# Kernel optimization log

Measured on AMD Instinct MI355X. Metric: run time of the kernel, lower is better.

The kernel has to match this reference:

```python
import jax, jax.numpy as jnp
import numpy as np
import math

PE_DIM = 96
MAX_LEN = 150

def make_pe():
    # deterministic sinusoidal position embedding buffer (requires_grad=False in torch)
    pe = np.zeros((MAX_LEN, PE_DIM), np.float32)
    pos = np.arange(MAX_LEN, dtype=np.float32)[:, None]
    div = np.exp(np.arange(0, PE_DIM, 2, dtype=np.float32) * (-math.log(10000.0) / PE_DIM))
    pe[:, 0::2] = np.sin(pos * div)
    pe[:, 1::2] = np.cos(pos * div)
    return jnp.asarray(pe)

def gru_cell(x, h, Wih, Whh, bih, bhh):
    # PyTorch GRU cell semantics
    gi = x @ Wih.T + bih            # [B, 3H]
    gh = h @ Whh.T + bhh            # [B, 3H]
    ir, iz, in_ = jnp.split(gi, 3, axis=-1)
    hr, hz, hn = jnp.split(gh, 3, axis=-1)
    r = jax.nn.sigmoid(ir + hr)
    z = jax.nn.sigmoid(iz + hz)
    n = jnp.tanh(in_ + r * hn)
    return (1.0 - z) * n + z * h

def gru_step(x, h, params):
    # x: [B, in], h: [L, B, H] -> (top-layer out [B,H], new h [L,B,H])
    hs = []
    inp = x
    for l, (Wih, Whh, bih, bhh) in enumerate(params):
        hn = gru_cell(inp, h[l], Wih, Whh, bih, bhh)
        hs.append(hn)
        inp = hn
    return inp, jnp.stack(hs)

def setup_inputs() -> dict:
    key = jax.random.key(0)
    ks = jax.random.split(key, 12)
    T, B, F, H = 50, 256, 96, 512
    rnn_in = 2 * F + PE_DIM  # 288
    k = 1.0 / math.sqrt(H)
    u = lambda kk, shp: jax.random.uniform(kk, shp, jnp.float32, -k, k)
    return {
        'input': jax.random.normal(ks[0], (T, B, F), jnp.float32),
        'W_ih0': u(ks[1], (3 * H, rnn_in)), 'W_hh0': u(ks[2], (3 * H, H)),
        'b_ih0': u(ks[3], (3 * H,)), 'b_hh0': u(ks[4], (3 * H,)),
        'W_ih1': u(ks[5], (3 * H, H)), 'W_hh1': u(ks[6], (3 * H, H)),
        'b_ih1': u(ks[7], (3 * H,)), 'b_hh1': u(ks[8], (3 * H,)),
        'W_lin': u(ks[9], (F, H)), 'b_lin': u(ks[10], (F,)),
    }

def reference(input, W_ih0, W_hh0, b_ih0, b_hh0, W_ih1, W_hh1, b_ih1, b_hh1, W_lin, b_lin):
    pe = make_pe()
    params = [(W_ih0, W_hh0, b_ih0, b_hh0), (W_ih1, W_hh1, b_ih1, b_hh1)]
    T, B, F = input.shape
    H = W_hh0.shape[1]
    # std mask: torch.std over time (unbiased) > 1e-4, shape [1,B,F]
    mask = (jnp.std(input, axis=0, ddof=1, keepdims=True) > 1e-4).astype(input.dtype)
    # ---- encoder ----
    vel = jnp.concatenate([jnp.zeros((1, B, F), input.dtype), input[1:] - input[:-1]], 0)
    pos = jnp.broadcast_to(pe[:T, None, :], (T, B, PE_DIM))
    x_en = jnp.concatenate([input, vel, pos], -1)  # [T,B,288]
    h0 = jnp.zeros((2, B, H), input.dtype)
    def enc_step(h, xt):
        out, hn = gru_step(xt, h, params)
        return hn, out
    h_en, outs = jax.lax.scan(enc_step, h0, x_en)
    outputs_enc = outs @ W_lin.T + b_lin + input  # residual: pred_pre = input
    pe_dec = pe[T:2 * T]  # step i uses pe[T+i]
    m = mask[0]
    def dec_core(prev_pred, vel_t, pe_t, h):
        x = jnp.concatenate([prev_pred, vel_t,
                             jnp.broadcast_to(pe_t[None, :], (B, PE_DIM))], -1)
        out, hn = gru_step(x, h, params)
        pred = (out @ W_lin.T + b_lin + prev_pred) * m  # residual then std_mask
        return pred, hn
    # step 0: input[0] with velocity input[0]-input[-1], hidden from encoder
    pred0, h = dec_core(input[0], input[0] - input[-1], pe_dec[0], h_en)
    # steps >=1: inp_cur = pred, and pred - outputs_dec[i-1] == 0 (faithful to source)
    zero_vel = jnp.zeros((B, F), input.dtype)
    def dec_step(carry, pe_t):
        pred, h = carry
        pred_n, hn = dec_core(pred, zero_vel, pe_t, h)
        return (pred_n, hn), pred_n
    _, preds = jax.lax.scan(dec_step, (pred0, h), pe_dec[1:])
    outputs_dec = jnp.concatenate([pred0[None], preds], 0)
    return (outputs_enc, outputs_dec)
```

## Files before the change

### kernel.cpp

```cpp
#include <hip/hip_runtime.h>
#include <math.h>

#define TT 50
#define BB 256
#define FF 96
#define HH 512
#define G3 1536
#define RNN_IN 288
#define HSZ (BB * HH)

typedef __attribute__((ext_vector_type(8))) short bhalf8;
typedef __attribute__((ext_vector_type(4))) float floatx4;
#define MFMA16 __builtin_amdgcn_mfma_f32_16x16x32_bf16

__device__ inline ushort f2bf(float f) {
    union { float f; unsigned u; } v; v.f = f;
    unsigned r = (v.u + 0x7FFFu + ((v.u >> 16) & 1u)) >> 16;
    return (ushort)r;
}
__device__ inline float bf2f(ushort h) {
    union { unsigned u; float f; } v; v.u = ((unsigned)h) << 16; return v.f;
}
__device__ inline bhalf8 ld8(const ushort* p) { return *(const bhalf8*)p; }
__device__ inline float sigmoidf_(float x) { return 1.f / (1.f + __expf(-x)); }

__device__ inline float pe_val(int pos, int d) {
    float dv = expf(-9.210340371976184f * (float)(d & ~1) / 96.0f);
    float a = (float)pos * dv;
    return (d & 1) ? cosf(a) : sinf(a);
}

__global__ __launch_bounds__(256) void prep_weights(
    const float* Wih0, const float* Whh0, const float* Wih1, const float* Whh1, const float* Wlin,
    ushort* dWih0, ushort* dWhh0, ushort* dWih1, ushort* dWhh1, ushort* dWlin)
{
    const int n0 = G3 * RNN_IN;
    const int n1 = G3 * HH;
    const int n2 = FF * HH;
    const int total = n0 + 3 * n1 + n2;
    for (int i = blockIdx.x * 256 + threadIdx.x; i < total; i += gridDim.x * 256) {
        int j = i;
        if (j < n0) { dWih0[j] = f2bf(Wih0[j]); continue; }
        j -= n0;
        if (j < n1) { dWhh0[j] = f2bf(Whh0[j]); continue; }
        j -= n1;
        if (j < n1) { dWih1[j] = f2bf(Wih1[j]); continue; }
        j -= n1;
        if (j < n1) { dWhh1[j] = f2bf(Whh1[j]); continue; }
        j -= n1;
        dWlin[j] = f2bf(Wlin[j]);
    }
}

__global__ __launch_bounds__(256) void prep_misc(
    const float* __restrict__ input, float* pe, float* maskp, ushort* x_en,
    ushort* hb, unsigned* bar)
{
    int i = blockIdx.x * 256 + threadIdx.x;
    if (i < TT * BB * RNN_IN) {
        int t = i / (BB * RNN_IN);
        int r = i % (BB * RNN_IN);
        int b = r / RNN_IN, c = r % RNN_IN;
        float v;
        if (c < FF) v = input[(t * BB + b) * FF + c];
        else if (c < 2 * FF) {
            int cc = c - FF;
            v = (t == 0) ? 0.f : input[(t * BB + b) * FF + cc] - input[((t - 1) * BB + b) * FF + cc];
        } else v = pe_val(t, c - 2 * FF);
        x_en[i] = f2bf(v);
        return;
    }
    i -= TT * BB * RNN_IN;
    if (i < BB * FF) {
        int b = i / FF, f = i % FF;
        float mean = 0.f, sq = 0.f;
        for (int t = 0; t < TT; t++) {
            float x = input[(t * BB + b) * FF + f];
            mean += x; sq += x * x;
        }
        mean /= (float)TT;
        float var = (sq - (float)TT * mean * mean) / (float)(TT - 1);
        float sd = sqrtf(fmaxf(var, 0.f));
        maskp[i] = (sd > 1e-4f) ? 1.f : 0.f;
        return;
    }
    i -= BB * FF;
    if (i < 100 * FF) { pe[i] = pe_val(i / FF, i % FF); return; }
    i -= 100 * FF;
    if (i < 4 * BB * HH) { hb[i] = 0; return; }
    i -= 4 * BB * HH;
    if (i < 16384) { bar[i] = 0; return; }
}

__global__ __launch_bounds__(256) void zpe_kernel(
    const float* __restrict__ pe, const float* __restrict__ Wih0,
    const float* __restrict__ bih0, float* __restrict__ Zpe)
{
    int idx = blockIdx.x * 256 + threadIdx.x;
    if (idx >= TT * G3) return;
    int t = idx / G3, n = idx % G3;
    float s = bih0[n];
    const float* per = pe + (TT + t) * FF;
    const float* wr = Wih0 + n * RNN_IN + 2 * FF;
    for (int k = 0; k < FF; k++) s += per[k] * wr[k];
    Zpe[idx] = s;
}

__global__ __launch_bounds__(256) void zvel_kernel(
    const float* __restrict__ input, const float* __restrict__ Wih0, float* __restrict__ Zvel)
{
    int idx = blockIdx.x * 256 + threadIdx.x;
    if (idx >= BB * G3) return;
    int m = idx / G3, n = idx % G3;
    const float* a0 = input + m * FF;
    const float* aL = input + (TT - 1) * BB * FF + m * FF;
    const float* wr = Wih0 + n * RNN_IN;
    float s = 0.f;
    for (int k = 0; k < FF; k++) s += a0[k] * wr[k] + (a0[k] - aL[k]) * wr[FF + k];
    Zvel[idx] = s;
}

__global__ __launch_bounds__(256) void gemm_z0(
    const ushort* __restrict__ A, const ushort* __restrict__ W,
    const float* __restrict__ bias, ushort* __restrict__ C)
{
    int lane = threadIdx.x & 63, w = threadIdx.x >> 6;
    int row0 = blockIdx.x * 64 + w * 16;
    int c0 = blockIdx.y * 96;
    int l15 = lane & 15, q = lane >> 4;
    const ushort* ap = A + (size_t)(row0 + l15) * RNN_IN + q * 8;
    floatx4 acc[6] = {};
    const ushort* wp[6];
#pragma unroll
    for (int j = 0; j < 6; j++) wp[j] = W + (size_t)(c0 + 16 * j + l15) * RNN_IN + q * 8;
    for (int kt = 0; kt < RNN_IN / 32; kt++) {
        bhalf8 a = ld8(ap + kt * 32);
#pragma unroll
        for (int j = 0; j < 6; j++) {
            bhalf8 b = ld8(wp[j] + kt * 32);
            acc[j] = MFMA16(a, b, acc[j], 0, 0, 0);
        }
    }
#pragma unroll
    for (int j = 0; j < 6; j++) {
        int col = c0 + 16 * j + l15;
        float bb = bias[col];
#pragma unroll
        for (int i = 0; i < 4; i++) {
            int r = row0 + q * 4 + i;
            C[(size_t)r * G3 + col] = f2bf(acc[j][i] + bb);
        }
    }
}

__global__ __launch_bounds__(256) void gemm_out_enc(
    const ushort* __restrict__ A, const ushort* __restrict__ W,
    const float* __restrict__ bias, const float* __restrict__ addsrc, float* __restrict__ out)
{
    int lane = threadIdx.x & 63, w = threadIdx.x >> 6;
    int row0 = blockIdx.x * 64 + w * 16;
    int l15 = lane & 15, q = lane >> 4;
    const ushort* ap = A + (size_t)(row0 + l15) * HH + q * 8;
    floatx4 acc[6] = {};
    const ushort* wp[6];
#pragma unroll
    for (int j = 0; j < 6; j++) wp[j] = W + (size_t)(16 * j + l15) * HH + q * 8;
    for (int kt = 0; kt < HH / 32; kt++) {
        bhalf8 a = ld8(ap + kt * 32);
#pragma unroll
        for (int j = 0; j < 6; j++) {
            bhalf8 b = ld8(wp[j] + kt * 32);
            acc[j] = MFMA16(a, b, acc[j], 0, 0, 0);
        }
    }
#pragma unroll
    for (int j = 0; j < 6; j++) {
        int col = 16 * j + l15;
        float bb = bias[col];
#pragma unroll
        for (int i = 0; i < 4; i++) {
            int r = row0 + q * 4 + i;
            out[(size_t)r * FF + col] = acc[j][i] + bb + addsrc[(size_t)r * FF + col];
        }
    }
}


struct PArgs {
    const ushort* Z0;
    const ushort* Wih0b;
    const ushort* Whh0b; const ushort* Wih1b; const ushort* Whh1b;
    const ushort* Wlinb;
    const float* bhh0; const float* bih1; const float* bhh1; const float* blin;
    const float* Zpe;
    const float* Zvel;
    const float* maskp;
    const float* input;
    ushort* h0buf;
    ushort* h1buf;
    ushort* outs;
    float* out;
    unsigned* slots;
};

__global__ __launch_bounds__(128) void persistent11(PArgs P)
{
    const int tid = threadIdx.x;
    const int w = tid >> 6;
    const int lane = tid & 63;
    const int l15 = lane & 15, q = lane >> 4;
    const int rg = blockIdx.x >> 4, cg = blockIdx.x & 15;
    const int row0 = rg * 16;
    const int ct = cg * 32 + w * 16;
    const int bcol = ct + q * 4;
    const int lcol = w * 16 + q * 4;

    __shared__ ushort h0stage[8192];
    __shared__ ushort h1stage[8192];
    __shared__ float h0f[16][36];
    __shared__ float h1f[16][36];
    __shared__ float predf[16][100];
    __shared__ float maskl[16][100];
    __shared__ ushort predb[16][104];

    for (int i = tid; i < 16 * 36; i += 128) { ((float*)h0f)[i] = 0.f; ((float*)h1f)[i] = 0.f; }
    for (int i = tid; i < 16 * 96; i += 128) {
        int r = i / 96, c = i % 96;
        float p0 = P.input[(row0 + r) * FF + c];
        predf[r][c] = p0;
        predb[r][c] = f2bf(p0);
        maskl[r][c] = P.maskp[(row0 + r) * FF + c];
    }
    __syncthreads();

    unsigned phase = 0;
    unsigned* myslot = P.slots + (size_t)(rg * 16 + cg) * 64;
    const unsigned* pslot = P.slots + (size_t)(rg * 16 + (tid & 15)) * 64;

    auto release = [&]() {
        phase++;
        asm volatile("s_waitcnt vmcnt(0)" ::: "memory");
        __syncthreads();
        if (tid == 0)
            __hip_atomic_store(myslot, phase, __ATOMIC_RELAXED, __HIP_MEMORY_SCOPE_AGENT);
    };
    auto wait_ = [&]() {
        if (tid < 16 && tid != cg) {
            while (__hip_atomic_load(pslot, __ATOMIC_RELAXED, __HIP_MEMORY_SCOPE_AGENT) < phase)
                __builtin_amdgcn_s_sleep(1);
        }
        __syncthreads();
        asm volatile("" ::: "memory");
    };

    auto stage = [&](const ushort* src, ushort* dst) {
        const int r = tid & 15;
        const int cb = tid >> 4;
        const unsigned long long* gp =
            (const unsigned long long*)(src + (size_t)(row0 + r) * HH + cb * 64);
        unsigned long long v[16];
#pragma unroll
        for (int j = 0; j < 16; j++)
            v[j] = __hip_atomic_load(gp + j, __ATOMIC_RELAXED, __HIP_MEMORY_SCOPE_AGENT);
#pragma unroll
        for (int qq = 0; qq < 8; qq++) {
            unsigned long long* lp = (unsigned long long*)(dst + ((cb * 8 + qq) * 16 + r) * 8);
            lp[0] = v[2 * qq];
            lp[1] = v[2 * qq + 1];
        }
    };

    auto gemm3_lds = [&](const ushort* hst, const ushort* W, floatx4 acc[3]) {
        const ushort* a0 = W + (size_t)(0 * HH + ct + l15) * HH + q * 8;
        const ushort* a1 = W + (size_t)(1 * HH + ct + l15) * HH + q * 8;
        const ushort* a2 = W + (size_t)(2 * HH + ct + l15) * HH + q * 8;
        for (int kt = 0; kt < 16; kt++) {
            bhalf8 b = *(const bhalf8*)&hst[((kt * 4 + q) * 16 + l15) * 8];
            acc[0] = MFMA16(ld8(a0), b, acc[0], 0, 0, 0); a0 += 32;
            acc[1] = MFMA16(ld8(a1), b, acc[1], 0, 0, 0); a1 += 32;
            acc[2] = MFMA16(ld8(a2), b, acc[2], 0, 0, 0); a2 += 32;
        }
    };

    auto gru_epi = [&](const floatx4 gi[3], const floatx4 gh[3], const float* bhh,
                       float (*hfl)[36], ushort* hnb, ushort* outs_t) {
        float4 bh_r = *(const float4*)&bhh[0 * HH + bcol];
        float4 bh_z = *(const float4*)&bhh[1 * HH + bcol];
        float4 bh_n = *(const float4*)&bhh[2 * HH + bcol];
        union { ushort s4[4]; unsigned long long u; } pk;
        const float* bhr = &bh_r.x; const float* bhz = &bh_z.x; const float* bhn = &bh_n.x;
#pragma unroll
        for (int i = 0; i < 4; i++) {
            float rg_ = sigmoidf_(gi[0][i] + gh[0][i] + bhr[i]);
            float zg = sigmoidf_(gi[1][i] + gh[1][i] + bhz[i]);
            float ng = tanhf(gi[2][i] + rg_ * (gh[2][i] + bhn[i]));
            float hn = (1.f - zg) * ng + zg * hfl[l15][lcol + i];
            hfl[l15][lcol + i] = hn;
            pk.s4[i] = f2bf(hn);
        }
        __hip_atomic_store((unsigned long long*)(hnb + (size_t)(row0 + l15) * HH + bcol), pk.u,
                           __ATOMIC_RELAXED, __HIP_MEMORY_SCOPE_AGENT);
        if (outs_t) *(unsigned long long*)(outs_t + (size_t)(row0 + l15) * HH + bcol) = pk.u;
    };

    auto pred_part = [&](int tpred) {
        float* outt = P.out + (size_t)(TT + tpred) * BB * FF;
        for (int jt = w; jt < 6; jt += 2) {
            floatx4 pa = {};
            const ushort* apw = P.Wlinb + (size_t)(jt * 16 + l15) * HH + q * 8;
            for (int kt = 0; kt < 16; kt++) {
                bhalf8 b = *(const bhalf8*)&h1stage[((kt * 4 + q) * 16 + l15) * 8];
                pa = MFMA16(ld8(apw), b, pa, 0, 0, 0); apw += 32;
            }
            int fc = jt * 16 + q * 4;
            float4 bl = *(const float4*)&P.blin[fc];
            const float* blp = &bl.x;
            float4 vout;
            float* vo = &vout.x;
#pragma unroll
            for (int i = 0; i < 4; i++) {
                float v = pa[i] + blp[i] + predf[l15][fc + i];
                v *= maskl[l15][fc + i];
                predf[l15][fc + i] = v;
                predb[l15][fc + i] = f2bf(v);
                vo[i] = v;
            }
            if (cg == 0) *(float4*)&outt[(size_t)(row0 + l15) * FF + fc] = vout;
        }
    };

    for (int s = 0; s <= TT; s++) {
        release();
        floatx4 gh1[3] = {};
        floatx4 gi0z[3];
        if (s >= 1) {
            stage(P.h1buf + (1 - (s & 1)) * HSZ, h1stage);
            __syncthreads();
            gemm3_lds(h1stage, P.Whh1b, gh1);
        }
        if (s < TT) {
            const ushort* zt = P.Z0 + ((size_t)s * BB + row0 + l15) * G3;
#pragma unroll
            for (int g = 0; g < 3; g++) {
                union { unsigned long long u; ushort s4[4]; } z;
                z.u = *(const unsigned long long*)(zt + g * HH + bcol);
#pragma unroll
                for (int i = 0; i < 4; i++) gi0z[g][i] = bf2f(z.s4[i]);
            }
        }
        wait_();
        stage(P.h0buf + (s & 1) * HSZ, h0stage);
        __syncthreads();
        if (s < TT) {
            floatx4 gh0[3] = {};
            gemm3_lds(h0stage, P.Whh0b, gh0);
            gru_epi(gi0z, gh0, P.bhh0, h0f, P.h0buf + (1 - (s & 1)) * HSZ, nullptr);
        }
        if (s >= 1) {
            int t = s - 1;
            floatx4 gi1[3] = {};
            gemm3_lds(h0stage, P.Wih1b, gi1);
            float4 bi0 = *(const float4*)&P.bih1[0 * HH + bcol];
            float4 bi1 = *(const float4*)&P.bih1[1 * HH + bcol];
            float4 bi2 = *(const float4*)&P.bih1[2 * HH + bcol];
            const float* b0 = &bi0.x; const float* b1 = &bi1.x; const float* b2 = &bi2.x;
#pragma unroll
            for (int i = 0; i < 4; i++) { gi1[0][i] += b0[i]; gi1[1][i] += b1[i]; gi1[2][i] += b2[i]; }
            gru_epi(gi1, gh1, P.bhh1, h1f, P.h1buf + (s & 1) * HSZ, P.outs + (size_t)t * BB * HH);
        }
    }

    for (int t = 0; t < TT; t++) {
        int pp = t & 1;
        release();
        stage(P.h0buf + pp * HSZ, h0stage);
        __syncthreads();
        floatx4 gh0[3] = {};
        gemm3_lds(h0stage, P.Whh0b, gh0);
        floatx4 zadd[3];
        {
            const float* zp = P.Zpe + (size_t)t * G3;
#pragma unroll
            for (int g = 0; g < 3; g++) {
                float4 z4 = *(const float4*)&zp[g * HH + bcol];
                const float* zp4 = &z4.x;
#pragma unroll
                for (int i = 0; i < 4; i++) zadd[g][i] = zp4[i];
            }
            if (t == 0) {
                const float* zv = P.Zvel + (size_t)(row0 + l15) * G3;
#pragma unroll
                for (int g = 0; g < 3; g++) {
                    float4 z4 = *(const float4*)&zv[g * HH + bcol];
                    const float* zp4 = &z4.x;
#pragma unroll
                    for (int i = 0; i < 4; i++) zadd[g][i] += zp4[i];
                }
            }
        }
        wait_();
        stage(P.h1buf + pp * HSZ, h1stage);
        __syncthreads();
        if (t > 0) {
            pred_part(t - 1);
            __syncthreads();
        }
        {
            floatx4 gi0[3] = {};
            if (t > 0) {
                const ushort* a0 = P.Wih0b + (size_t)(0 * HH + ct + l15) * RNN_IN + q * 8;
                const ushort* a1 = P.Wih0b + (size_t)(1 * HH + ct + l15) * RNN_IN + q * 8;
                const ushort* a2 = P.Wih0b + (size_t)(2 * HH + ct + l15) * RNN_IN + q * 8;
                for (int kt = 0; kt < 3; kt++) {
                    bhalf8 b = *(const bhalf8*)(&predb[l15][kt * 32 + q * 8]);
                    gi0[0] = MFMA16(ld8(a0), b, gi0[0], 0, 0, 0); a0 += 32;
                    gi0[1] = MFMA16(ld8(a1), b, gi0[1], 0, 0, 0); a1 += 32;
                    gi0[2] = MFMA16(ld8(a2), b, gi0[2], 0, 0, 0); a2 += 32;
                }
            }
#pragma unroll
            for (int g = 0; g < 3; g++)
#pragma unroll
                for (int i = 0; i < 4; i++) gi0[g][i] += zadd[g][i];
            gru_epi(gi0, gh0, P.bhh0, h0f, P.h0buf + (1 - pp) * HSZ, nullptr);
        }

        release();
        floatx4 gh1[3] = {};
        gemm3_lds(h1stage, P.Whh1b, gh1);
        wait_();
        stage(P.h0buf + (1 - pp) * HSZ, h0stage);
        __syncthreads();
        {
            floatx4 gi1[3] = {};
            gemm3_lds(h0stage, P.Wih1b, gi1);
            float4 bi0 = *(const float4*)&P.bih1[0 * HH + bcol];
            float4 bi1 = *(const float4*)&P.bih1[1 * HH + bcol];
            float4 bi2 = *(const float4*)&P.bih1[2 * HH + bcol];
            const float* b0 = &bi0.x; const float* b1 = &bi1.x; const float* b2 = &bi2.x;
#pragma unroll
            for (int i = 0; i < 4; i++) { gi1[0][i] += b0[i]; gi1[1][i] += b1[i]; gi1[2][i] += b2[i]; }
            gru_epi(gi1, gh1, P.bhh1, h1f, P.h1buf + (1 - pp) * HSZ, nullptr);
        }
    }
    release();
    wait_();
    stage(P.h1buf + 0 * HSZ, h1stage);
    __syncthreads();
    pred_part(TT - 1);
}

extern "C" void kernel_launch(void* const* d_in, const int* in_sizes, int n_in,
                              void* d_out, int out_size, void* d_ws, size_t ws_size,
                              hipStream_t stream)
{
    const float* input = (const float*)d_in[0];
    const float* W_ih0 = (const float*)d_in[1];
    const float* W_hh0 = (const float*)d_in[2];
    const float* b_ih0 = (const float*)d_in[3];
    const float* b_hh0 = (const float*)d_in[4];
    const float* W_ih1 = (const float*)d_in[5];
    const float* W_hh1 = (const float*)d_in[6];
    const float* b_ih1 = (const float*)d_in[7];
    const float* b_hh1 = (const float*)d_in[8];
    const float* W_lin = (const float*)d_in[9];
    const float* b_lin = (const float*)d_in[10];
    float* out = (float*)d_out;

    char* ws = (char*)d_ws;
    size_t off = 0;
    auto alloc = [&](size_t bytes) -> char* {
        off = (off + 255) & ~(size_t)255;
        char* p = ws + off;
        off += bytes;
        return p;
    };

    ushort* Wih0b = (ushort*)alloc((size_t)G3 * RNN_IN * 2);
    ushort* Whh0b = (ushort*)alloc((size_t)G3 * HH * 2);
    ushort* Wih1b = (ushort*)alloc((size_t)G3 * HH * 2);
    ushort* Whh1b = (ushort*)alloc((size_t)G3 * HH * 2);
    ushort* Wlinb = (ushort*)alloc((size_t)FF * HH * 2);
    ushort* x_en  = (ushort*)alloc((size_t)TT * BB * RNN_IN * 2);
    ushort* Z0    = (ushort*)alloc((size_t)TT * BB * G3 * 2);
    ushort* outs  = (ushort*)alloc((size_t)TT * BB * HH * 2);
    float*  Zpe   = (float*)alloc((size_t)TT * G3 * 4);
    float*  Zvel  = (float*)alloc((size_t)BB * G3 * 4);
    float*  pe    = (float*)alloc((size_t)100 * FF * 4);
    float*  maskp = (float*)alloc((size_t)BB * FF * 4);
    ushort* hb    = (ushort*)alloc((size_t)4 * BB * HH * 2);
    unsigned* bar = (unsigned*)alloc(16384 * 4);
    (void)ws_size; (void)in_sizes; (void)n_in; (void)out_size;

    dim3 blk(256);

    prep_weights<<<dim3(512), blk, 0, stream>>>(W_ih0, W_hh0, W_ih1, W_hh1, W_lin,
                                                Wih0b, Whh0b, Wih1b, Whh1b, Wlinb);
    {
        int total = TT * BB * RNN_IN + BB * FF + 100 * FF + 4 * BB * HH + 16384;
        prep_misc<<<dim3((total + 255) / 256), blk, 0, stream>>>(
            input, pe, maskp, x_en, hb, bar);
    }
    gemm_z0<<<dim3(TT * BB / 64, G3 / 96), blk, 0, stream>>>(x_en, Wih0b, b_ih0, Z0);
    zpe_kernel<<<dim3((TT * G3 + 255) / 256), blk, 0, stream>>>(pe, W_ih0, b_ih0, Zpe);
    zvel_kernel<<<dim3((BB * G3 + 255) / 256), blk, 0, stream>>>(input, W_ih0, Zvel);

    PArgs P;
    P.Z0 = Z0; P.Wih0b = Wih0b; P.Whh0b = Whh0b; P.Wih1b = Wih1b; P.Whh1b = Whh1b; P.Wlinb = Wlinb;
    P.bhh0 = b_hh0; P.bih1 = b_ih1; P.bhh1 = b_hh1; P.blin = b_lin;
    P.Zpe = Zpe; P.Zvel = Zvel; P.maskp = maskp; P.input = input;
    P.h0buf = hb; P.h1buf = hb + 2 * HSZ;
    P.outs = outs; P.out = out; P.slots = bar;

    void* kargs[] = { &P };
    hipError_t e = hipLaunchCooperativeKernel((void*)persistent11, dim3(256), dim3(128), kargs, 0, stream);
    (void)e;

    gemm_out_enc<<<dim3(TT * BB / 64, 1), blk, 0, stream>>>(outs, Wlinb, b_lin, input, out);
}
```

Before: 2.078 ms.

## Double block size and split layer-0/layer-1 GRU work across wave pairs

The persistent cooperative kernel moves from 128 to 256 threads per block. Waves 0-1 now handle layer-0 work (Whh0, Wih0, Z loads) and waves 2-3 handle layer-1 work (Whh1, Wih1, prediction), so the two layers' GEMMs run concurrently within each step rather than one after another. LDS staging is spread across twice as many threads. The cost is more registers and waves per CU and a few added block barriers.

```diff
diff --git a/kernel.cpp b/kernel.cpp
--- a/kernel.cpp
+++ b/kernel.cpp
@@ -203,17 +203,19 @@
     unsigned* slots;
 };
 
-__global__ __launch_bounds__(128) void persistent11(PArgs P)
+__global__ __launch_bounds__(256) void persistent12(PArgs P)
 {
     const int tid = threadIdx.x;
     const int w = tid >> 6;
+    const int wp = w >> 1;
+    const int wi = w & 1;
     const int lane = tid & 63;
     const int l15 = lane & 15, q = lane >> 4;
     const int rg = blockIdx.x >> 4, cg = blockIdx.x & 15;
     const int row0 = rg * 16;
-    const int ct = cg * 32 + w * 16;
+    const int ct = cg * 32 + wi * 16;
     const int bcol = ct + q * 4;
-    const int lcol = w * 16 + q * 4;
+    const int lcol = wi * 16 + q * 4;
 
     __shared__ ushort h0stage[8192];
     __shared__ ushort h1stage[8192];
@@ -223,8 +225,8 @@
     __shared__ float maskl[16][100];
     __shared__ ushort predb[16][104];
 
-    for (int i = tid; i < 16 * 36; i += 128) { ((float*)h0f)[i] = 0.f; ((float*)h1f)[i] = 0.f; }
-    for (int i = tid; i < 16 * 96; i += 128) {
+    for (int i = tid; i < 16 * 36; i += 256) { ((float*)h0f)[i] = 0.f; ((float*)h1f)[i] = 0.f; }
+    for (int i = tid; i < 16 * 96; i += 256) {
         int r = i / 96, c = i % 96;
         float p0 = P.input[(row0 + r) * FF + c];
         predf[r][c] = p0;
@@ -257,14 +259,14 @@
         const int r = tid & 15;
         const int cb = tid >> 4;
         const unsigned long long* gp =
-            (const unsigned long long*)(src + (size_t)(row0 + r) * HH + cb * 64);
-        unsigned long long v[16];
-#pragma unroll
-        for (int j = 0; j < 16; j++)
+            (const unsigned long long*)(src + (size_t)(row0 + r) * HH + cb * 32);
+        unsigned long long v[8];
+#pragma unroll
+        for (int j = 0; j < 8; j++)
             v[j] = __hip_atomic_load(gp + j, __ATOMIC_RELAXED, __HIP_MEMORY_SCOPE_AGENT);
 #pragma unroll
-        for (int qq = 0; qq < 8; qq++) {
-            unsigned long long* lp = (unsigned long long*)(dst + ((cb * 8 + qq) * 16 + r) * 8);
+        for (int qq = 0; qq < 4; qq++) {
+            unsigned long long* lp = (unsigned long long*)(dst + ((cb * 4 + qq) * 16 + r) * 8);
             lp[0] = v[2 * qq];
             lp[1] = v[2 * qq + 1];
         }
@@ -305,7 +307,7 @@
 
     auto pred_part = [&](int tpred) {
         float* outt = P.out + (size_t)(TT + tpred) * BB * FF;
-        for (int jt = w; jt < 6; jt += 2) {
+        for (int jt = wi; jt < 6; jt += 2) {
             floatx4 pa = {};
             const ushort* apw = P.Wlinb + (size_t)(jt * 16 + l15) * HH + q * 8;
             for (int kt = 0; kt < 16; kt++) {
@@ -331,14 +333,12 @@
 
     for (int s = 0; s <= TT; s++) {
         release();
+        if (s >= 1) stage(P.h1buf + (1 - (s & 1)) * HSZ, h1stage);
+        __syncthreads();
         floatx4 gh1[3] = {};
         floatx4 gi0z[3];
-        if (s >= 1) {
-            stage(P.h1buf + (1 - (s & 1)) * HSZ, h1stage);
-            __syncthreads();
-            gemm3_lds(h1stage, P.Whh1b, gh1);
-        }
-        if (s < TT) {
+        if (wp == 1 && s >= 1) gemm3_lds(h1stage, P.Whh1b, gh1);
+        if (wp == 0 && s < TT) {
             const ushort* zt = P.Z0 + ((size_t)s * BB + row0 + l15) * G3;
 #pragma unroll
             for (int g = 0; g < 3; g++) {
@@ -351,12 +351,12 @@
         wait_();
         stage(P.h0buf + (s & 1) * HSZ, h0stage);
         __syncthreads();
-        if (s < TT) {
+        if (wp == 0 && s < TT) {
             floatx4 gh0[3] = {};
             gemm3_lds(h0stage, P.Whh0b, gh0);
             gru_epi(gi0z, gh0, P.bhh0, h0f, P.h0buf + (1 - (s & 1)) * HSZ, nullptr);
         }
-        if (s >= 1) {
+        if (wp == 1 && s >= 1) {
             int t = s - 1;
             floatx4 gi1[3] = {};
             gemm3_lds(h0stage, P.Wih1b, gi1);
@@ -375,10 +375,9 @@
         release();
         stage(P.h0buf + pp * HSZ, h0stage);
         __syncthreads();
-        floatx4 gh0[3] = {};
-        gemm3_lds(h0stage, P.Whh0b, gh0);
-        floatx4 zadd[3];
-        {
+        floatx4 gh0[3] = {}, zadd[3];
+        if (wp == 0) {
+            gemm3_lds(h0stage, P.Whh0b, gh0);
             const float* zp = P.Zpe + (size_t)t * G3;
 #pragma unroll
             for (int g = 0; g < 3; g++) {
@@ -402,10 +401,10 @@
         stage(P.h1buf + pp * HSZ, h1stage);
         __syncthreads();
         if (t > 0) {
-            pred_part(t - 1);
+            if (wp == 1) pred_part(t - 1);
             __syncthreads();
         }
-        {
+        if (wp == 0) {
             floatx4 gi0[3] = {};
             if (t > 0) {
                 const ushort* a0 = P.Wih0b + (size_t)(0 * HH + ct + l15) * RNN_IN + q * 8;
@@ -427,11 +426,11 @@
 
         release();
         floatx4 gh1[3] = {};
-        gemm3_lds(h1stage, P.Whh1b, gh1);
+        if (wp == 1) gemm3_lds(h1stage, P.Whh1b, gh1);
         wait_();
         stage(P.h0buf + (1 - pp) * HSZ, h0stage);
         __syncthreads();
-        {
+        if (wp == 1) {
             floatx4 gi1[3] = {};
             gemm3_lds(h0stage, P.Wih1b, gi1);
             float4 bi0 = *(const float4*)&P.bih1[0 * HH + bcol];
@@ -447,7 +446,7 @@
     wait_();
     stage(P.h1buf + 0 * HSZ, h1stage);
     __syncthreads();
-    pred_part(TT - 1);
+    if (wp == 1) pred_part(TT - 1);
 }
 
 extern "C" void kernel_launch(void* const* d_in, const int* in_sizes, int n_in,
@@ -513,7 +512,7 @@
     P.outs = outs; P.out = out; P.slots = bar;
 
     void* kargs[] = { &P };
-    hipError_t e = hipLaunchCooperativeKernel((void*)persistent11, dim3(256), dim3(128), kargs, 0, stream);
+    hipError_t e = hipLaunchCooperativeKernel((void*)persistent12, dim3(256), dim3(256), kargs, 0, stream);
     (void)e;
 
     gemm_out_enc<<<dim3(TT * BB / 64, 1), blk, 0, stream>>>(outs, Wlinb, b_lin, input, out);
```

Measured after the change: 1.891 ms. 9.0% less time.
